# Optimization experiments

Hardware: AMD Instinct MI355X
Metric: run time of the kernel (lower is better)

Reference implementation:

```python
import jax, jax.numpy as jnp
import numpy as np

INPUT_DIM1 = 512
INPUT_DIM2 = 512
OUTPUT_DIM = 8192


def _make_sketch(seed_h, seed_s, input_dim, output_dim):
    # Faithful to torch module: dense [input_dim, output_dim] matrix with one
    # nonzero (+-1) per row at column rand_h[i].
    np.random.seed(seed_h)
    rand_h = np.random.randint(output_dim, size=input_dim)
    np.random.seed(seed_s)
    rand_s = (2 * np.random.randint(2, size=input_dim) - 1).astype(np.float32)
    M = np.zeros((input_dim, output_dim), dtype=np.float32)
    M[np.arange(input_dim), rand_h] = rand_s
    return jnp.asarray(M)


def setup_inputs() -> dict:
    key = jax.random.key(0)
    k1, k2 = jax.random.split(key)
    bottom1 = jax.random.normal(k1, (32, INPUT_DIM1, 14, 14), dtype=jnp.float32)
    bottom2 = jax.random.normal(k2, (32, INPUT_DIM2, 14, 14), dtype=jnp.float32)
    S1 = _make_sketch(1, 3, INPUT_DIM1, OUTPUT_DIM)
    S2 = _make_sketch(5, 7, INPUT_DIM2, OUTPUT_DIM)
    return {"bottom1": bottom1, "bottom2": bottom2, "S1": S1, "S2": S2}


def reference(bottom1, bottom2, S1, S2):
    B, _, H, W = bottom1.shape
    d = S1.shape[1]
    # [B, C, H, W] -> [B*H*W, C]
    b1 = jnp.transpose(bottom1, (0, 2, 3, 1)).reshape(-1, bottom1.shape[1])
    b2 = jnp.transpose(bottom2, (0, 2, 3, 1)).reshape(-1, bottom2.shape[1])
    sketch1 = b1 @ S1  # [N, d]
    sketch2 = b2 @ S2
    fft1 = jnp.fft.fft(sketch1, axis=-1)
    fft2 = jnp.fft.fft(sketch2, axis=-1)
    cbp_flat = jnp.real(jnp.fft.ifft(fft1 * fft2, axis=-1))
    cbp = cbp_flat.reshape(B, H, W, d)
    return cbp.sum(axis=(1, 2))  # sum_pool=True -> [B, d]
```

## Files before the change

kernel.cpp:

```cpp
#include <hip/hip_runtime.h>


#define D     8192
#define DMASK 8191
#define C     512
#define HW    196
#define NB    32
#define LDK   40
#define NCH   7
#define NSL   16

typedef __attribute__((ext_vector_type(8))) short bf16x8;
typedef __attribute__((ext_vector_type(4))) float f32x4;

struct MTArr { unsigned v[C]; };

constexpr MTArr mt_draws(unsigned seed) {
    unsigned mt[624] = {};
    mt[0] = seed;
    for (int i = 1; i < 624; ++i)
        mt[i] = 1812433253u * (mt[i - 1] ^ (mt[i - 1] >> 30)) + (unsigned)i;
    for (int i = 0; i < 624; ++i) {
        const unsigned y = (mt[i] & 0x80000000u) | (mt[(i + 1) % 624] & 0x7fffffffu);
        mt[i] = mt[(i + 397) % 624] ^ (y >> 1) ^ ((y & 1u) ? 0x9908b0dfu : 0u);
    }
    MTArr out{};
    for (int i = 0; i < C; ++i) {
        unsigned y = mt[i];
        y ^= y >> 11;
        y ^= (y << 7)  & 0x9d2c5680u;
        y ^= (y << 15) & 0xefc60000u;
        y ^= y >> 18;
        out.v[i] = y;
    }
    return out;
}

__device__ constexpr MTArr MT_H1 = mt_draws(1);
__device__ constexpr MTArr MT_S1 = mt_draws(3);
__device__ constexpr MTArr MT_H2 = mt_draws(5);
__device__ constexpr MTArr MT_S2 = mt_draws(7);

__global__ __launch_bounds__(512) void extract_rng(
    const float* __restrict__ S1, const float* __restrict__ S2,
    int* __restrict__ h1, float* __restrict__ s1,
    int* __restrict__ h2, float* __restrict__ s2)
{
    const int  c     = threadIdx.x;
    const bool first = (blockIdx.x == 0);
    const float* S = first ? S1 : S2;

    int   h = (int)((first ? MT_H1.v[c] : MT_H2.v[c]) & (unsigned)DMASK);
    float s = (float)(2 * (int)((first ? MT_S1.v[c] : MT_S2.v[c]) & 1u) - 1);

    const float val = S[(size_t)c * D + h];
    if (val != s) {
        const float4* rp = (const float4*)(S + (size_t)c * D);
        for (int i = 0; i < D / 4; ++i) {
            float4 v = rp[i];
            if (v.x != 0.f) { h = 4 * i + 0; s = v.x; }
            if (v.y != 0.f) { h = 4 * i + 1; s = v.y; }
            if (v.z != 0.f) { h = 4 * i + 2; s = v.z; }
            if (v.w != 0.f) { h = 4 * i + 3; s = v.w; }
        }
    }
    if (first) { h1[c] = h; s1[c] = s; }
    else       { h2[c] = h; s2[c] = s; }
}

__device__ __forceinline__ unsigned short f2bf(float f, unsigned xm) {
    unsigned u = __float_as_uint(f) ^ xm;
    return (unsigned short)((u + 0x7fffu + ((u >> 16) & 1u)) >> 16);
}

__global__ __launch_bounds__(256, 2) void cbp_mfma(
    const float* __restrict__ b1, const float* __restrict__ b2,
    const int* __restrict__ h1, const float* __restrict__ s1,
    const int* __restrict__ h2, const float* __restrict__ s2,
    float* __restrict__ P)
{
    const int b  = blockIdx.z;
    const int t1 = blockIdx.y;
    const int t2 = blockIdx.x;

    __shared__ float hist[D];
    __shared__ __align__(16) unsigned short As[128 * LDK];
    __shared__ __align__(16) unsigned short Bs[128 * LDK];
    __shared__ int h1t[128], h2t[128];

    const int tid = threadIdx.x;

    #pragma unroll
    for (int i = 0; i < 8; ++i) {
        float4 z = {0.f, 0.f, 0.f, 0.f};
        ((float4*)hist)[tid + 256 * i] = z;
    }
    if (tid < 128) {
        h1t[tid] = h1[t1 * 128 + tid];
        h2t[tid] = h2[t2 * 128 + tid];
    }

    const int rr  = tid >> 3;
    const int kq4 = (tid & 7) * 4;

    const float* Abase = b1 + ((size_t)b * C + (size_t)t1 * 128) * HW;
    const float* Bbase = b2 + ((size_t)b * C + (size_t)t2 * 128) * HW;

    unsigned am[4], bm[4];
    #pragma unroll
    for (int ii = 0; ii < 4; ++ii) {
        am[ii] = (s1[t1 * 128 + rr + 32 * ii] < 0.f) ? 0x80000000u : 0u;
        bm[ii] = (s2[t2 * 128 + rr + 32 * ii] < 0.f) ? 0x80000000u : 0u;
    }

    float4 pva[4], pvb[4];
    #pragma unroll
    for (int ii = 0; ii < 4; ++ii) {
        pva[ii] = *(const float4*)(Abase + (size_t)(rr + 32 * ii) * HW + kq4);
        pvb[ii] = *(const float4*)(Bbase + (size_t)(rr + 32 * ii) * HW + kq4);
    }

    const int lane  = tid & 63;
    const int w     = tid >> 6;
    const int ln15  = lane & 15;
    const int qd    = lane >> 4;
    const int koff  = qd * 8;
    const int mbase = (w >> 1) * 64;
    const int nbase = (w & 1) * 64;

    f32x4 acc[4][4] = {};

    for (int ch = 0; ch < NCH; ++ch) {
        #pragma unroll
        for (int ii = 0; ii < 4; ++ii) {
            const int r = rr + 32 * ii;
            uint2 pa, pb;
            pa.x = (unsigned)f2bf(pva[ii].x, am[ii]) |
                   ((unsigned)f2bf(pva[ii].y, am[ii]) << 16);
            pa.y = (unsigned)f2bf(pva[ii].z, am[ii]) |
                   ((unsigned)f2bf(pva[ii].w, am[ii]) << 16);
            pb.x = (unsigned)f2bf(pvb[ii].x, bm[ii]) |
                   ((unsigned)f2bf(pvb[ii].y, bm[ii]) << 16);
            pb.y = (unsigned)f2bf(pvb[ii].z, bm[ii]) |
                   ((unsigned)f2bf(pvb[ii].w, bm[ii]) << 16);
            *(uint2*)&As[r * LDK + kq4] = pa;
            *(uint2*)&Bs[r * LDK + kq4] = pb;
        }
        __syncthreads();

        if (ch + 1 < NCH) {
            const int gk = (ch + 1) * 32 + kq4;
            const bool valid = (gk + 4 <= HW);
            const float4 z = {0.f, 0.f, 0.f, 0.f};
            #pragma unroll
            for (int ii = 0; ii < 4; ++ii) {
                pva[ii] = valid ? *(const float4*)(Abase + (size_t)(rr + 32 * ii) * HW + gk) : z;
                pvb[ii] = valid ? *(const float4*)(Bbase + (size_t)(rr + 32 * ii) * HW + gk) : z;
            }
        }

        bf16x8 av[4], bv[4];
        #pragma unroll
        for (int i = 0; i < 4; ++i)
            av[i] = *(const bf16x8*)&As[(mbase + i * 16 + ln15) * LDK + koff];
        #pragma unroll
        for (int j = 0; j < 4; ++j)
            bv[j] = *(const bf16x8*)&Bs[(nbase + j * 16 + ln15) * LDK + koff];
        #pragma unroll
        for (int i = 0; i < 4; ++i)
            #pragma unroll
            for (int j = 0; j < 4; ++j)
                acc[i][j] = __builtin_amdgcn_mfma_f32_16x16x32_bf16(
                    av[i], bv[j], acc[i][j], 0, 0, 0);
        __syncthreads();
    }

    int p1v[16];
    #pragma unroll
    for (int i = 0; i < 4; ++i)
        #pragma unroll
        for (int qq = 0; qq < 4; ++qq)
            p1v[i * 4 + qq] = h1t[mbase + i * 16 + qd * 4 + qq];
    int p2v[4];
    #pragma unroll
    for (int j = 0; j < 4; ++j)
        p2v[j] = h2t[nbase + j * 16 + ln15];

    #pragma unroll
    for (int i = 0; i < 4; ++i)
        #pragma unroll
        for (int j = 0; j < 4; ++j)
            #pragma unroll
            for (int qq = 0; qq < 4; ++qq)
                atomicAdd(&hist[(p1v[i * 4 + qq] + p2v[j]) & DMASK], acc[i][j][qq]);

    __syncthreads();

    float* Pslice = P + (size_t)(b * NSL + t1 * 4 + t2) * D;
    #pragma unroll
    for (int i = 0; i < 8; ++i)
        ((float4*)Pslice)[tid + 256 * i] = ((const float4*)hist)[tid + 256 * i];
}

__global__ __launch_bounds__(256) void reduce16(
    const float* __restrict__ P, float* __restrict__ out)
{
    const int idx4 = blockIdx.x * 256 + threadIdx.x;
    const int b    = idx4 >> 11;
    const int d4   = idx4 & 2047;

    const float4* base = (const float4*)(P + (size_t)b * NSL * D) + d4;
    float4 v[NSL];
    #pragma unroll
    for (int s = 0; s < NSL; ++s) v[s] = base[s * (D / 4)];

    float4 acc = v[0];
    #pragma unroll
    for (int s = 1; s < NSL; ++s) {
        acc.x += v[s].x; acc.y += v[s].y; acc.z += v[s].z; acc.w += v[s].w;
    }
    ((float4*)out)[idx4] = acc;
}

extern "C" void kernel_launch(void* const* d_in, const int* in_sizes, int n_in,
                              void* d_out, int out_size, void* d_ws, size_t ws_size,
                              hipStream_t stream)
{
    const float* bottom1 = (const float*)d_in[0];
    const float* bottom2 = (const float*)d_in[1];
    const float* S1      = (const float*)d_in[2];
    const float* S2      = (const float*)d_in[3];
    float* out = (float*)d_out;

    float* P  = (float*)d_ws;
    int*   h1 = (int*)(P + (size_t)NB * NSL * D);
    int*   h2 = h1 + C;
    float* s1 = (float*)(h2 + C);
    float* s2 = s1 + C;

    extract_rng<<<2, 512, 0, stream>>>(S1, S2, h1, s1, h2, s2);
    cbp_mfma<<<dim3(4, 4, NB), 256, 0, stream>>>(bottom1, bottom2,
                                                 h1, s1, h2, s2, P);
    reduce16<<<256, 256, 0, stream>>>(P, out);
}
```

Baseline: 148.7 us.

## Stage full K extent in LDS and drop per-chunk synchronization

Each block now loads its entire 128x196 slices of both inputs into shared memory as bf16 in one pass, then runs all MFMA K-steps without per-chunk barriers. The block grows to 512 threads with each wave computing a 32x64 tile, the grid is flattened to 1D, and histogram scatter uses unsafeAtomicAdd. This aims to remove the serialized load/convert/sync loop, at the cost of much larger LDS usage that limits blocks per CU.

```diff
diff --git a/kernel.cpp b/kernel.cpp
--- a/kernel.cpp
+++ b/kernel.cpp
@@ -6,7 +6,7 @@
 #define C     512
 #define HW    196
 #define NB    32
-#define LDK   40
+#define LDK2  232
 #define NCH   7
 #define NSL   16
 
@@ -73,133 +73,125 @@
     return (unsigned short)((u + 0x7fffu + ((u >> 16) & 1u)) >> 16);
 }
 
-__global__ __launch_bounds__(256, 2) void cbp_mfma(
+__device__ __forceinline__ uint2 pack4(float4 v, unsigned xm) {
+    uint2 u;
+    u.x = (unsigned)f2bf(v.x, xm) | ((unsigned)f2bf(v.y, xm) << 16);
+    u.y = (unsigned)f2bf(v.z, xm) | ((unsigned)f2bf(v.w, xm) << 16);
+    return u;
+}
+
+__global__ __launch_bounds__(512, 2) void cbp_mfma(
     const float* __restrict__ b1, const float* __restrict__ b2,
     const int* __restrict__ h1, const float* __restrict__ s1,
     const int* __restrict__ h2, const float* __restrict__ s2,
     float* __restrict__ P)
 {
-    const int b  = blockIdx.z;
-    const int t1 = blockIdx.y;
-    const int t2 = blockIdx.x;
+    const int id = blockIdx.x;
+    const int b  = id & 31;
+    const int m  = id >> 5;
+    const int t1 = m >> 2;
+    const int t2 = m & 3;
 
     __shared__ float hist[D];
-    __shared__ __align__(16) unsigned short As[128 * LDK];
-    __shared__ __align__(16) unsigned short Bs[128 * LDK];
+    __shared__ __align__(16) unsigned short As[128 * LDK2];
+    __shared__ __align__(16) unsigned short Bs[128 * LDK2];
     __shared__ int h1t[128], h2t[128];
 
     const int tid = threadIdx.x;
 
     #pragma unroll
-    for (int i = 0; i < 8; ++i) {
+    for (int i = 0; i < 4; ++i) {
         float4 z = {0.f, 0.f, 0.f, 0.f};
-        ((float4*)hist)[tid + 256 * i] = z;
+        ((float4*)hist)[tid + 512 * i] = z;
     }
     if (tid < 128) {
         h1t[tid] = h1[t1 * 128 + tid];
         h2t[tid] = h2[t2 * 128 + tid];
     }
 
-    const int rr  = tid >> 3;
-    const int kq4 = (tid & 7) * 4;
-
-    const float* Abase = b1 + ((size_t)b * C + (size_t)t1 * 128) * HW;
-    const float* Bbase = b2 + ((size_t)b * C + (size_t)t2 * 128) * HW;
-
-    unsigned am[4], bm[4];
-    #pragma unroll
-    for (int ii = 0; ii < 4; ++ii) {
-        am[ii] = (s1[t1 * 128 + rr + 32 * ii] < 0.f) ? 0x80000000u : 0u;
-        bm[ii] = (s2[t2 * 128 + rr + 32 * ii] < 0.f) ? 0x80000000u : 0u;
-    }
-
-    float4 pva[4], pvb[4];
-    #pragma unroll
-    for (int ii = 0; ii < 4; ++ii) {
-        pva[ii] = *(const float4*)(Abase + (size_t)(rr + 32 * ii) * HW + kq4);
-        pvb[ii] = *(const float4*)(Bbase + (size_t)(rr + 32 * ii) * HW + kq4);
-    }
+    const int r = tid >> 2;
+    const int q = tid & 3;
+
+    const float4* Arow = (const float4*)(b1 + ((size_t)b * C + t1 * 128 + r) * HW);
+    const float4* Brow = (const float4*)(b2 + ((size_t)b * C + t2 * 128 + r) * HW);
+    const unsigned am = (s1[t1 * 128 + r] < 0.f) ? 0x80000000u : 0u;
+    const unsigned bm = (s2[t2 * 128 + r] < 0.f) ? 0x80000000u : 0u;
+
+    float4 va[13], vb[13];
+    #pragma unroll
+    for (int t = 0; t < 13; ++t) {
+        const int j = q + 4 * t;
+        if (j < 49) { va[t] = Arow[j]; vb[t] = Brow[j]; }
+    }
+    unsigned short* ArL = &As[r * LDK2];
+    unsigned short* BrL = &Bs[r * LDK2];
+    #pragma unroll
+    for (int t = 0; t < 13; ++t) {
+        const int j = q + 4 * t;
+        if (j < 49) {
+            *(uint2*)&ArL[4 * j] = pack4(va[t], am);
+            *(uint2*)&BrL[4 * j] = pack4(vb[t], bm);
+        }
+    }
+    if (q == 1) {
+        const uint2 z2 = {0u, 0u};
+        #pragma unroll
+        for (int t = 0; t < 9; ++t) {
+            *(uint2*)&ArL[196 + 4 * t] = z2;
+            *(uint2*)&BrL[196 + 4 * t] = z2;
+        }
+    }
+    __syncthreads();
 
     const int lane  = tid & 63;
     const int w     = tid >> 6;
     const int ln15  = lane & 15;
     const int qd    = lane >> 4;
     const int koff  = qd * 8;
-    const int mbase = (w >> 1) * 64;
+    const int mbase = (w >> 1) * 32;
     const int nbase = (w & 1) * 64;
 
-    f32x4 acc[4][4] = {};
-
+    f32x4 acc[2][4] = {};
+
+    #pragma unroll
     for (int ch = 0; ch < NCH; ++ch) {
-        #pragma unroll
-        for (int ii = 0; ii < 4; ++ii) {
-            const int r = rr + 32 * ii;
-            uint2 pa, pb;
-            pa.x = (unsigned)f2bf(pva[ii].x, am[ii]) |
-                   ((unsigned)f2bf(pva[ii].y, am[ii]) << 16);
-            pa.y = (unsigned)f2bf(pva[ii].z, am[ii]) |
-                   ((unsigned)f2bf(pva[ii].w, am[ii]) << 16);
-            pb.x = (unsigned)f2bf(pvb[ii].x, bm[ii]) |
-                   ((unsigned)f2bf(pvb[ii].y, bm[ii]) << 16);
-            pb.y = (unsigned)f2bf(pvb[ii].z, bm[ii]) |
-                   ((unsigned)f2bf(pvb[ii].w, bm[ii]) << 16);
-            *(uint2*)&As[r * LDK + kq4] = pa;
-            *(uint2*)&Bs[r * LDK + kq4] = pb;
-        }
-        __syncthreads();
-
-        if (ch + 1 < NCH) {
-            const int gk = (ch + 1) * 32 + kq4;
-            const bool valid = (gk + 4 <= HW);
-            const float4 z = {0.f, 0.f, 0.f, 0.f};
-            #pragma unroll
-            for (int ii = 0; ii < 4; ++ii) {
-                pva[ii] = valid ? *(const float4*)(Abase + (size_t)(rr + 32 * ii) * HW + gk) : z;
-                pvb[ii] = valid ? *(const float4*)(Bbase + (size_t)(rr + 32 * ii) * HW + gk) : z;
-            }
-        }
-
-        bf16x8 av[4], bv[4];
-        #pragma unroll
-        for (int i = 0; i < 4; ++i)
-            av[i] = *(const bf16x8*)&As[(mbase + i * 16 + ln15) * LDK + koff];
+        const int kk = ch * 32 + koff;
+        bf16x8 av[2], bv[4];
+        #pragma unroll
+        for (int i = 0; i < 2; ++i)
+            av[i] = *(const bf16x8*)&As[(mbase + i * 16 + ln15) * LDK2 + kk];
         #pragma unroll
         for (int j = 0; j < 4; ++j)
-            bv[j] = *(const bf16x8*)&Bs[(nbase + j * 16 + ln15) * LDK + koff];
-        #pragma unroll
-        for (int i = 0; i < 4; ++i)
+            bv[j] = *(const bf16x8*)&Bs[(nbase + j * 16 + ln15) * LDK2 + kk];
+        #pragma unroll
+        for (int i = 0; i < 2; ++i)
             #pragma unroll
             for (int j = 0; j < 4; ++j)
                 acc[i][j] = __builtin_amdgcn_mfma_f32_16x16x32_bf16(
                     av[i], bv[j], acc[i][j], 0, 0, 0);
-        __syncthreads();
-    }
-
-    int p1v[16];
-    #pragma unroll
-    for (int i = 0; i < 4; ++i)
-        #pragma unroll
-        for (int qq = 0; qq < 4; ++qq)
-            p1v[i * 4 + qq] = h1t[mbase + i * 16 + qd * 4 + qq];
+    }
+
     int p2v[4];
     #pragma unroll
     for (int j = 0; j < 4; ++j)
         p2v[j] = h2t[nbase + j * 16 + ln15];
 
     #pragma unroll
+    for (int i = 0; i < 2; ++i)
+        #pragma unroll
+        for (int qq = 0; qq < 4; ++qq) {
+            const int p1 = h1t[mbase + i * 16 + qd * 4 + qq];
+            #pragma unroll
+            for (int j = 0; j < 4; ++j)
+                unsafeAtomicAdd(&hist[(p1 + p2v[j]) & DMASK], acc[i][j][qq]);
+        }
+
+    __syncthreads();
+
+    float* Pslice = P + (size_t)(b * NSL + t1 * 4 + t2) * D;
+    #pragma unroll
     for (int i = 0; i < 4; ++i)
-        #pragma unroll
-        for (int j = 0; j < 4; ++j)
-            #pragma unroll
-            for (int qq = 0; qq < 4; ++qq)
-                atomicAdd(&hist[(p1v[i * 4 + qq] + p2v[j]) & DMASK], acc[i][j][qq]);
-
-    __syncthreads();
-
-    float* Pslice = P + (size_t)(b * NSL + t1 * 4 + t2) * D;
-    #pragma unroll
-    for (int i = 0; i < 8; ++i)
-        ((float4*)Pslice)[tid + 256 * i] = ((const float4*)hist)[tid + 256 * i];
+        ((float4*)Pslice)[tid + 512 * i] = ((const float4*)hist)[tid + 512 * i];
 }
 
 __global__ __launch_bounds__(256) void reduce16(
@@ -239,7 +231,7 @@
     float* s2 = s1 + C;
 
     extract_rng<<<2, 512, 0, stream>>>(S1, S2, h1, s1, h2, s2);
-    cbp_mfma<<<dim3(4, 4, NB), 256, 0, stream>>>(bottom1, bottom2,
-                                                 h1, s1, h2, s2, P);
+    cbp_mfma<<<512, 512, 0, stream>>>(bottom1, bottom2,
+                                      h1, s1, h2, s2, P);
     reduce16<<<256, 256, 0, stream>>>(P, out);
 }
```

New measurement: 150.5 us. About the same (+1.2%).

## Stream fp32 tiles into LDS via async DMA with double buffering

Applied to the files above, without the earlier changes.

The GEMM-histogram kernel now copies fp32 input tiles straight from global memory into double-buffered, XOR-swizzled shared memory using global_load_lds, instead of staging them through registers and converting to bf16 before the store. The bf16 conversion and sign flip move to fragment-build time using the hardware bf16x2 conversion. The 4-element K tail is handled separately in registers, which drops one barrier per chunk. The change also remaps blocks to a 1D grid with the batch index in the low bits, and switches LDS atomics to unsafeAtomicAdd. Shared memory use grows a lot (fp32 and double-buffered), which may reduce occupancy. Conversion work is repeated per fragment read rather than done once per element.

```diff
diff --git a/kernel.cpp b/kernel.cpp
--- a/kernel.cpp
+++ b/kernel.cpp
@@ -1,4 +1,5 @@
 #include <hip/hip_runtime.h>
+#include <hip/hip_bf16.h>
 
 
 #define D     8192
@@ -6,8 +7,7 @@
 #define C     512
 #define HW    196
 #define NB    32
-#define LDK   40
-#define NCH   7
+#define NCH2  6
 #define NSL   16
 
 typedef __attribute__((ext_vector_type(8))) short bf16x8;
@@ -68,27 +68,47 @@
     else       { h2[c] = h; s2[c] = s; }
 }
 
-__device__ __forceinline__ unsigned short f2bf(float f, unsigned xm) {
-    unsigned u = __float_as_uint(f) ^ xm;
-    return (unsigned short)((u + 0x7fffu + ((u >> 16) & 1u)) >> 16);
-}
-
-__global__ __launch_bounds__(256, 2) void cbp_mfma(
+__device__ __forceinline__ unsigned cvt2(float a, float b) {
+    __hip_bfloat162 h = __float22bfloat162_rn(make_float2(a, b));
+    return *(unsigned*)&h;
+}
+
+__device__ __forceinline__ bf16x8 mkfrag(const float* __restrict__ buf,
+                                         int row, int q0, int r7, unsigned msk) {
+    const float4 f0 = *(const float4*)&buf[row * 32 + (((q0)     ^ r7) * 4)];
+    const float4 f1 = *(const float4*)&buf[row * 32 + (((q0 + 1) ^ r7) * 4)];
+    union { unsigned u[4]; bf16x8 v; } r;
+    r.u[0] = cvt2(f0.x, f0.y) ^ msk;
+    r.u[1] = cvt2(f0.z, f0.w) ^ msk;
+    r.u[2] = cvt2(f1.x, f1.y) ^ msk;
+    r.u[3] = cvt2(f1.z, f1.w) ^ msk;
+    return r.v;
+}
+
+#define DMA16(GP, LP) __builtin_amdgcn_global_load_lds( \
+    (const __attribute__((address_space(1))) void*)(GP), \
+    (__attribute__((address_space(3))) void*)(LP), 16, 0, 0)
+
+__global__ __launch_bounds__(256) void cbp_dma(
     const float* __restrict__ b1, const float* __restrict__ b2,
     const int* __restrict__ h1, const float* __restrict__ s1,
     const int* __restrict__ h2, const float* __restrict__ s2,
     float* __restrict__ P)
 {
-    const int b  = blockIdx.z;
-    const int t1 = blockIdx.y;
-    const int t2 = blockIdx.x;
+    const int id = blockIdx.x;
+    const int b  = id & 31;
+    const int m  = id >> 5;
+    const int t1 = m >> 2;
+    const int t2 = m & 3;
 
     __shared__ float hist[D];
-    __shared__ __align__(16) unsigned short As[128 * LDK];
-    __shared__ __align__(16) unsigned short Bs[128 * LDK];
+    __shared__ __align__(16) float Af[2][128 * 32];
+    __shared__ __align__(16) float Bf[2][128 * 32];
     __shared__ int h1t[128], h2t[128];
 
-    const int tid = threadIdx.x;
+    const int tid  = threadIdx.x;
+    const int lane = tid & 63;
+    const int w    = tid >> 6;
 
     #pragma unroll
     for (int i = 0; i < 8; ++i) {
@@ -100,79 +120,95 @@
         h2t[tid] = h2[t2 * 128 + tid];
     }
 
-    const int rr  = tid >> 3;
-    const int kq4 = (tid & 7) * 4;
-
-    const float* Abase = b1 + ((size_t)b * C + (size_t)t1 * 128) * HW;
-    const float* Bbase = b2 + ((size_t)b * C + (size_t)t2 * 128) * HW;
-
-    unsigned am[4], bm[4];
-    #pragma unroll
-    for (int ii = 0; ii < 4; ++ii) {
-        am[ii] = (s1[t1 * 128 + rr + 32 * ii] < 0.f) ? 0x80000000u : 0u;
-        bm[ii] = (s2[t2 * 128 + rr + 32 * ii] < 0.f) ? 0x80000000u : 0u;
-    }
-
-    float4 pva[4], pvb[4];
-    #pragma unroll
-    for (int ii = 0; ii < 4; ++ii) {
-        pva[ii] = *(const float4*)(Abase + (size_t)(rr + 32 * ii) * HW + kq4);
-        pvb[ii] = *(const float4*)(Bbase + (size_t)(rr + 32 * ii) * HW + kq4);
-    }
-
-    const int lane  = tid & 63;
-    const int w     = tid >> 6;
+    const int rl   = lane >> 3;
+    const int slot = lane & 7;
+    const int gk0  = (slot ^ rl) * 4;
+
+    const float* Apl = b1 + ((size_t)b * C + t1 * 128 + w * 32 + rl) * HW + gk0;
+    const float* Bpl = b2 + ((size_t)b * C + t2 * 128 + w * 32 + rl) * HW + gk0;
+
+    #pragma unroll
+    for (int t = 0; t < 4; ++t) {
+        DMA16(Apl + (size_t)t * 8 * HW, &Af[0][(w * 32 + t * 8) * 32]);
+        DMA16(Bpl + (size_t)t * 8 * HW, &Bf[0][(w * 32 + t * 8) * 32]);
+    }
+
     const int ln15  = lane & 15;
     const int qd    = lane >> 4;
-    const int koff  = qd * 8;
+    const int r7    = ln15 & 7;
+    const int q0    = qd * 2;
     const int mbase = (w >> 1) * 64;
     const int nbase = (w & 1) * 64;
 
+    unsigned amk[4], bmk[4];
+    float4 ta[4], tb[4];
+    #pragma unroll
+    for (int i = 0; i < 4; ++i) {
+        const int ra = t1 * 128 + mbase + i * 16 + ln15;
+        const int rb = t2 * 128 + nbase + i * 16 + ln15;
+        amk[i] = (s1[ra] < 0.f) ? 0x80008000u : 0u;
+        bmk[i] = (s2[rb] < 0.f) ? 0x80008000u : 0u;
+        if (qd == 0) {
+            ta[i] = *(const float4*)(b1 + ((size_t)b * C + ra) * HW + 192);
+            tb[i] = *(const float4*)(b2 + ((size_t)b * C + rb) * HW + 192);
+        }
+    }
+
     f32x4 acc[4][4] = {};
-
-    for (int ch = 0; ch < NCH; ++ch) {
-        #pragma unroll
-        for (int ii = 0; ii < 4; ++ii) {
-            const int r = rr + 32 * ii;
-            uint2 pa, pb;
-            pa.x = (unsigned)f2bf(pva[ii].x, am[ii]) |
-                   ((unsigned)f2bf(pva[ii].y, am[ii]) << 16);
-            pa.y = (unsigned)f2bf(pva[ii].z, am[ii]) |
-                   ((unsigned)f2bf(pva[ii].w, am[ii]) << 16);
-            pb.x = (unsigned)f2bf(pvb[ii].x, bm[ii]) |
-                   ((unsigned)f2bf(pvb[ii].y, bm[ii]) << 16);
-            pb.y = (unsigned)f2bf(pvb[ii].z, bm[ii]) |
-                   ((unsigned)f2bf(pvb[ii].w, bm[ii]) << 16);
-            *(uint2*)&As[r * LDK + kq4] = pa;
-            *(uint2*)&Bs[r * LDK + kq4] = pb;
-        }
+    int buf = 0;
+
+    for (int ch = 0; ch < NCH2; ++ch) {
         __syncthreads();
 
-        if (ch + 1 < NCH) {
-            const int gk = (ch + 1) * 32 + kq4;
-            const bool valid = (gk + 4 <= HW);
-            const float4 z = {0.f, 0.f, 0.f, 0.f};
-            #pragma unroll
-            for (int ii = 0; ii < 4; ++ii) {
-                pva[ii] = valid ? *(const float4*)(Abase + (size_t)(rr + 32 * ii) * HW + gk) : z;
-                pvb[ii] = valid ? *(const float4*)(Bbase + (size_t)(rr + 32 * ii) * HW + gk) : z;
+        if (ch + 1 < NCH2) {
+            const int ko = (ch + 1) * 32;
+            #pragma unroll
+            for (int t = 0; t < 4; ++t) {
+                DMA16(Apl + ko + (size_t)t * 8 * HW, &Af[buf ^ 1][(w * 32 + t * 8) * 32]);
+                DMA16(Bpl + ko + (size_t)t * 8 * HW, &Bf[buf ^ 1][(w * 32 + t * 8) * 32]);
             }
         }
 
+        const float* Ab = Af[buf];
+        const float* Bb = Bf[buf];
         bf16x8 av[4], bv[4];
         #pragma unroll
         for (int i = 0; i < 4; ++i)
-            av[i] = *(const bf16x8*)&As[(mbase + i * 16 + ln15) * LDK + koff];
+            av[i] = mkfrag(Ab, mbase + i * 16 + ln15, q0, r7, amk[i]);
         #pragma unroll
         for (int j = 0; j < 4; ++j)
-            bv[j] = *(const bf16x8*)&Bs[(nbase + j * 16 + ln15) * LDK + koff];
+            bv[j] = mkfrag(Bb, nbase + j * 16 + ln15, q0, r7, bmk[j]);
         #pragma unroll
         for (int i = 0; i < 4; ++i)
             #pragma unroll
             for (int j = 0; j < 4; ++j)
                 acc[i][j] = __builtin_amdgcn_mfma_f32_16x16x32_bf16(
                     av[i], bv[j], acc[i][j], 0, 0, 0);
-        __syncthreads();
+        buf ^= 1;
+    }
+
+    {
+        bf16x8 av[4], bv[4];
+        #pragma unroll
+        for (int i = 0; i < 4; ++i) {
+            union { unsigned u[4]; bf16x8 v; } ra, rb;
+            if (qd == 0) {
+                ra.u[0] = cvt2(ta[i].x, ta[i].y) ^ amk[i];
+                ra.u[1] = cvt2(ta[i].z, ta[i].w) ^ amk[i];
+                rb.u[0] = cvt2(tb[i].x, tb[i].y) ^ bmk[i];
+                rb.u[1] = cvt2(tb[i].z, tb[i].w) ^ bmk[i];
+            } else {
+                ra.u[0] = 0u; ra.u[1] = 0u; rb.u[0] = 0u; rb.u[1] = 0u;
+            }
+            ra.u[2] = 0u; ra.u[3] = 0u; rb.u[2] = 0u; rb.u[3] = 0u;
+            av[i] = ra.v; bv[i] = rb.v;
+        }
+        #pragma unroll
+        for (int i = 0; i < 4; ++i)
+            #pragma unroll
+            for (int j = 0; j < 4; ++j)
+                acc[i][j] = __builtin_amdgcn_mfma_f32_16x16x32_bf16(
+                    av[i], bv[j], acc[i][j], 0, 0, 0);
     }
 
     int p1v[16];
@@ -192,11 +228,12 @@
         for (int j = 0; j < 4; ++j)
             #pragma unroll
             for (int qq = 0; qq < 4; ++qq)
-                atomicAdd(&hist[(p1v[i * 4 + qq] + p2v[j]) & DMASK], acc[i][j][qq]);
+                unsafeAtomicAdd(&hist[(p1v[i * 4 + qq] + p2v[j]) & DMASK],
+                                acc[i][j][qq]);
 
     __syncthreads();
 
-    float* Pslice = P + (size_t)(b * NSL + t1 * 4 + t2) * D;
+    float* Pslice = P + (size_t)(b * NSL + m) * D;
     #pragma unroll
     for (int i = 0; i < 8; ++i)
         ((float4*)Pslice)[tid + 256 * i] = ((const float4*)hist)[tid + 256 * i];
@@ -239,7 +276,6 @@
     float* s2 = s1 + C;
 
     extract_rng<<<2, 512, 0, stream>>>(S1, S2, h1, s1, h2, s2);
-    cbp_mfma<<<dim3(4, 4, NB), 256, 0, stream>>>(bottom1, bottom2,
-                                                 h1, s1, h2, s2, P);
+    cbp_dma<<<512, 256, 0, stream>>>(bottom1, bottom2, h1, s1, h2, s2, P);
     reduce16<<<256, 256, 0, stream>>>(P, out);
 }
```

After: 161.4 us. 1.09x slower.
